# Optimization experiments

Hardware: AMD Instinct MI355X
Metric: run time of the kernel (lower is better)

Reference implementation:

```python
import jax, jax.numpy as jnp
import numpy as np

B, S, HIDDEN = 1, 2048, 2048
NUM_HEADS, MLA_DIM = 16, 128
HEAD_DIM = HIDDEN // NUM_HEADS
ROPE_BASE = 10000.0


def setup_inputs() -> dict:
    key = jax.random.key(0)
    ks = jax.random.split(key, 5)
    sd = 0.02
    hidden_states = jax.random.normal(ks[0], (B, S, HIDDEN), dtype=jnp.float32)
    wq = jax.random.normal(ks[1], (HIDDEN, NUM_HEADS * MLA_DIM), dtype=jnp.float32) * sd
    wk = jax.random.normal(ks[2], (HIDDEN, NUM_HEADS * MLA_DIM), dtype=jnp.float32) * sd
    wv = jax.random.normal(ks[3], (HIDDEN, HIDDEN), dtype=jnp.float32) * sd
    wo = jax.random.normal(ks[4], (HIDDEN, HIDDEN), dtype=jnp.float32) * sd
    # causal additive mask [B, 1, S, S]
    causal = jnp.tril(jnp.ones((S, S), dtype=bool))
    attention_mask = jnp.where(causal, 0.0, -1e9).astype(jnp.float32)[None, None]
    attention_mask = jnp.broadcast_to(attention_mask, (B, 1, S, S))
    return {"hidden_states": hidden_states, "wq": wq, "wk": wk, "wv": wv,
            "wo": wo, "attention_mask": attention_mask}


def _rope_cos_sin(seq_len, dim, dtype):
    inv_freq = 1.0 / (ROPE_BASE ** (jnp.arange(0, dim, 2, dtype=jnp.float32) / dim))
    t = jnp.arange(seq_len, dtype=jnp.float32)
    freqs = jnp.einsum('i,j->ij', t, inv_freq)           # [S, dim/2]
    emb = jnp.concatenate([freqs, freqs], axis=-1)       # [S, dim]
    cos = jnp.cos(emb)[None, :, None, :].astype(dtype)   # [1, S, 1, dim]
    sin = jnp.sin(emb)[None, :, None, :].astype(dtype)
    return cos, sin


def _rotate_half(x):
    x1, x2 = jnp.split(x, 2, axis=-1)
    return jnp.concatenate([-x2, x1], axis=-1)


def reference(hidden_states, wq, wk, wv, wo, attention_mask):
    b, s, _ = hidden_states.shape
    q = (hidden_states @ wq).reshape(b, s, NUM_HEADS, MLA_DIM)
    k = (hidden_states @ wk).reshape(b, s, NUM_HEADS, MLA_DIM)
    v = (hidden_states @ wv).reshape(b, s, NUM_HEADS, HEAD_DIM)
    cos, sin = _rope_cos_sin(s, MLA_DIM, q.dtype)
    q = q * cos + _rotate_half(q) * sin
    k = k * cos + _rotate_half(k) * sin
    scale = 1.0 / np.sqrt(MLA_DIM)
    scores = jnp.einsum('bqhd,bkhd->bhqk', q, k) * scale + attention_mask
    probs = jax.nn.softmax(scores, axis=-1)
    out = jnp.einsum('bhqk,bkhd->bqhd', probs, v).reshape(b, s, HIDDEN)
    return out @ wo
```

## Files before the change

kernel.cpp:

```cpp
#include <hip/hip_runtime.h>
#include <math.h>

namespace {

constexpr int SEQ = 2048;
constexpr int HID = 2048;
constexpr int NH  = 16;
constexpr int DH  = 128;

using f32x4  = __attribute__((ext_vector_type(4))) float;
using short8 = __attribute__((ext_vector_type(8))) short;

__device__ __forceinline__ float bflo(unsigned u) { return __uint_as_float(u << 16); }
__device__ __forceinline__ float bfhi(unsigned u) { return __uint_as_float(u & 0xFFFF0000u); }
__device__ __forceinline__ unsigned short f2bf(float f) {
    unsigned u = __float_as_uint(f);
    u += 0x7FFFu + ((u >> 16) & 1u);
    return (unsigned short)(u >> 16);
}

typedef const __attribute__((address_space(1))) unsigned int GUI;
typedef __attribute__((address_space(3))) unsigned int LUI;
__device__ __forceinline__ void async16(const void* g, void* l) {
    __builtin_amdgcn_global_load_lds((GUI*)g, (LUI*)l, 16, 0, 0);
}

__global__ __launch_bounds__(256)
void cast_bf16(const float* __restrict__ X, unsigned short* __restrict__ Y)
{
    const int i = blockIdx.x * 256 + threadIdx.x;
    const float4 v = reinterpret_cast<const float4*>(X)[i];
    ushort4 o;
    o.x = f2bf(v.x); o.y = f2bf(v.y); o.z = f2bf(v.z); o.w = f2bf(v.w);
    reinterpret_cast<ushort4*>(Y)[i] = o;
}

__global__ __launch_bounds__(256)
void transpose_cast3(const float* __restrict__ w0, const float* __restrict__ w1,
                     const float* __restrict__ w2, unsigned short* __restrict__ WT3)
{
    const int z = blockIdx.z;
    const float* W = (z == 0) ? w0 : (z == 1) ? w1 : w2;
    unsigned short* WT = WT3 + (size_t)z * HID * HID;

    __shared__ float t[32][66];
    const int tx = threadIdx.x & 31, ty = threadIdx.x >> 5;
    const int n0 = blockIdx.x * 64, k0 = blockIdx.y * 32;
    #pragma unroll
    for (int i = 0; i < 4; ++i) {
        const int kr = ty + 8 * i;
        const float2 v = *reinterpret_cast<const float2*>(
            &W[(size_t)(k0 + kr) * HID + n0 + 2 * tx]);
        t[kr][2 * tx]     = v.x;
        t[kr][2 * tx + 1] = v.y;
    }
    __syncthreads();
    #pragma unroll
    for (int i = 0; i < 8; ++i) {
        const int n = ty + 8 * i;
        WT[(size_t)(n0 + n) * HID + k0 + tx] = f2bf(t[tx][n]);
    }
}

__global__ __launch_bounds__(256)
void transpose_cast(const float* __restrict__ W, unsigned short* __restrict__ WT)
{
    __shared__ float t[32][66];
    const int tx = threadIdx.x & 31, ty = threadIdx.x >> 5;
    const int n0 = blockIdx.x * 64, k0 = blockIdx.y * 32;
    #pragma unroll
    for (int i = 0; i < 4; ++i) {
        const int kr = ty + 8 * i;
        const float2 v = *reinterpret_cast<const float2*>(
            &W[(size_t)(k0 + kr) * HID + n0 + 2 * tx]);
        t[kr][2 * tx]     = v.x;
        t[kr][2 * tx + 1] = v.y;
    }
    __syncthreads();
    #pragma unroll
    for (int i = 0; i < 8; ++i) {
        const int n = ty + 8 * i;
        WT[(size_t)(n0 + n) * HID + k0 + tx] = f2bf(t[tx][n]);
    }
}

__global__ __launch_bounds__(256)
void transp_bf16(const unsigned short* __restrict__ X, unsigned short* __restrict__ Y)
{
    __shared__ unsigned short t[32][34];
    const int tx = threadIdx.x & 31, ty = threadIdx.x >> 5;
    const int i0 = blockIdx.y * 32, j0 = blockIdx.x * 32;
    #pragma unroll
    for (int q = 0; q < 4; ++q)
        t[ty + 8 * q][tx] = X[(size_t)(i0 + ty + 8 * q) * HID + j0 + tx];
    __syncthreads();
    #pragma unroll
    for (int q = 0; q < 4; ++q)
        Y[(size_t)(j0 + ty + 8 * q) * HID + i0 + tx] = t[tx][ty + 8 * q];
}

__global__ __launch_bounds__(256)
void gemm_qkv(const unsigned short* __restrict__ A,
              const unsigned short* __restrict__ Bt3,
              unsigned short* __restrict__ Qo,
              unsigned short* __restrict__ Ko,
              unsigned short* __restrict__ Vo)
{
    __shared__ unsigned short As[128 * 64];
    __shared__ unsigned short Bs[128 * 64];

    const int tid  = threadIdx.x;
    const int lane = tid & 63;
    const int w    = tid >> 6;
    const int wr   = w >> 1, wc = w & 1;

    const int b  = blockIdx.x;
    const int sw = (b & 7) * 96 + (b >> 3);
    const int mt = sw & 15, nt = sw >> 4;
    const int m0  = mt * 128;
    const int n0g = nt * 128;
    const int wi  = nt >> 4;
    const int n0  = (nt & 15) * 128;
    unsigned short* C = (wi == 0) ? Qo : (wi == 1) ? Ko : Vo;

    const int srow = lane >> 3;
    const int sunit = lane & 7;
    const int cl = lane & 15, lg = lane >> 4;

    f32x4 acc[4][4] = {};

    for (int k0 = 0; k0 < HID; k0 += 64) {
        __syncthreads();
        #pragma unroll
        for (int i = 0; i < 4; ++i) {
            const int rb = (w * 4 + i) * 8;
            const int r  = rb + srow;
            async16(A   + (size_t)(m0  + r) * HID + k0 + sunit * 8, &As[rb * 64]);
            async16(Bt3 + (size_t)(n0g + r) * HID + k0 + sunit * 8, &Bs[rb * 64]);
        }
        __syncthreads();

        #pragma unroll
        for (int ks = 0; ks < 2; ++ks) {
            short8 af[4], bf[4];
            #pragma unroll
            for (int i = 0; i < 4; ++i) {
                af[i] = *reinterpret_cast<const short8*>(
                    &As[(wr * 64 + i * 16 + cl) * 64 + ks * 32 + lg * 8]);
                bf[i] = *reinterpret_cast<const short8*>(
                    &Bs[(wc * 64 + i * 16 + cl) * 64 + ks * 32 + lg * 8]);
            }
            #pragma unroll
            for (int i = 0; i < 4; ++i)
                #pragma unroll
                for (int j = 0; j < 4; ++j)
                    acc[i][j] = __builtin_amdgcn_mfma_f32_16x16x32_bf16(
                        af[i], bf[j], acc[i][j], 0, 0, 0);
        }
    }

    const int rg = lg * 4;
    #pragma unroll
    for (int i = 0; i < 4; ++i)
        #pragma unroll
        for (int j = 0; j < 4; ++j)
            #pragma unroll
            for (int rr = 0; rr < 4; ++rr) {
                const int row = m0 + wr * 64 + i * 16 + rg + rr;
                const int col = n0 + wc * 64 + j * 16 + cl;
                C[(size_t)row * HID + col] = f2bf(acc[i][j][rr]);
            }
}

__global__ __launch_bounds__(256)
void gemm_wo_sk(const unsigned short* __restrict__ A,
                const unsigned short* __restrict__ Bt,
                float* __restrict__ P0, float* __restrict__ P1)
{
    __shared__ unsigned short As[128 * 64];
    __shared__ unsigned short Bs[128 * 64];

    const int tid  = threadIdx.x;
    const int lane = tid & 63;
    const int w    = tid >> 6;
    const int wr   = w >> 1, wc = w & 1;

    const int b     = blockIdx.x;
    const int chunk = b >> 8;
    const int bb    = b & 255;
    const int sw = (bb & 7) * 32 + (bb >> 3);
    const int m0 = (sw >> 4) * 128, n0 = (sw & 15) * 128;
    float* C = chunk ? P1 : P0;
    const int kbase = chunk * 1024;

    const int srow = lane >> 3;
    const int sunit = lane & 7;
    const int cl = lane & 15, lg = lane >> 4;

    f32x4 acc[4][4] = {};

    for (int k0 = 0; k0 < 1024; k0 += 64) {
        __syncthreads();
        #pragma unroll
        for (int i = 0; i < 4; ++i) {
            const int rb = (w * 4 + i) * 8;
            const int r  = rb + srow;
            async16(A  + (size_t)(m0 + r) * HID + kbase + k0 + sunit * 8, &As[rb * 64]);
            async16(Bt + (size_t)(n0 + r) * HID + kbase + k0 + sunit * 8, &Bs[rb * 64]);
        }
        __syncthreads();

        #pragma unroll
        for (int ks = 0; ks < 2; ++ks) {
            short8 af[4], bf[4];
            #pragma unroll
            for (int i = 0; i < 4; ++i) {
                af[i] = *reinterpret_cast<const short8*>(
                    &As[(wr * 64 + i * 16 + cl) * 64 + ks * 32 + lg * 8]);
                bf[i] = *reinterpret_cast<const short8*>(
                    &Bs[(wc * 64 + i * 16 + cl) * 64 + ks * 32 + lg * 8]);
            }
            #pragma unroll
            for (int i = 0; i < 4; ++i)
                #pragma unroll
                for (int j = 0; j < 4; ++j)
                    acc[i][j] = __builtin_amdgcn_mfma_f32_16x16x32_bf16(
                        af[i], bf[j], acc[i][j], 0, 0, 0);
        }
    }

    const int rg = lg * 4;
    #pragma unroll
    for (int i = 0; i < 4; ++i)
        #pragma unroll
        for (int j = 0; j < 4; ++j)
            #pragma unroll
            for (int rr = 0; rr < 4; ++rr) {
                const int row = m0 + wr * 64 + i * 16 + rg + rr;
                const int col = n0 + wc * 64 + j * 16 + cl;
                C[(size_t)row * HID + col] = acc[i][j][rr];
            }
}

__global__ __launch_bounds__(256)
void reduce2(const float* __restrict__ P0, const float* __restrict__ P1,
             float* __restrict__ out)
{
    const int i = blockIdx.x * 256 + threadIdx.x;
    const float4 a = reinterpret_cast<const float4*>(P0)[i];
    const float4 b = reinterpret_cast<const float4*>(P1)[i];
    float4 r; r.x = a.x + b.x; r.y = a.y + b.y; r.z = a.z + b.z; r.w = a.w + b.w;
    reinterpret_cast<float4*>(out)[i] = r;
}

__global__ __launch_bounds__(256)
void rope_qk(unsigned short* __restrict__ Q, unsigned short* __restrict__ K)
{
    const int idx = blockIdx.x * 256 + threadIdx.x;
    const int d = idx & 63;
    const int h = (idx >> 6) & (NH - 1);
    const int s = idx >> 10;

    const float invf = exp2f(-(float)d * (13.287712379549449f / 64.0f));
    float sn, c;
    sincosf((float)s * invf, &sn, &c);

    const float SC = 0.08838834764831845f;
    const size_t base = (size_t)s * HID + h * DH + d;

    const float a0 = __uint_as_float((unsigned)Q[base]      << 16);
    const float a1 = __uint_as_float((unsigned)Q[base + 64] << 16);
    Q[base]      = f2bf((a0 * c - a1 * sn) * SC);
    Q[base + 64] = f2bf((a1 * c + a0 * sn) * SC);
    const float b0 = __uint_as_float((unsigned)K[base]      << 16);
    const float b1 = __uint_as_float((unsigned)K[base + 64] << 16);
    K[base]      = f2bf(b0 * c - b1 * sn);
    K[base + 64] = f2bf(b1 * c + b0 * sn);
}

__global__ __launch_bounds__(512, 4)
void attn_part(const unsigned short* __restrict__ Q,
               const unsigned short* __restrict__ K,
               const unsigned short* __restrict__ Vt,
               unsigned short* __restrict__ Opart,
               float2* __restrict__ ML,
               unsigned short* __restrict__ AO)
{
    __shared__ unsigned short Ks[64 * 128];
    __shared__ unsigned short Vs[128 * 64];
    __shared__ unsigned short Ps[8][16 * 72];

    const int tid  = threadIdx.x;
    const int lane = tid & 63;
    const int w    = tid >> 6;

    const int h = blockIdx.x / 30;
    int c = blockIdx.x - h * 30;
    int qb = 0;
    while (true) {
        const int cnt = (qb + 6) / 6;
        if (c < cnt) break;
        c -= cnt; ++qb;
    }
    const int cnt = (qb + 6) / 6;
    const int q0 = qb * 128;
    const int t0 = c * 12;
    const int t1 = min(2 * (qb + 1), t0 + 12);
    const bool direct = (cnt == 1);
    const int pidx = h * 24 + ((qb < 12) ? (qb - 6) * 2 : 12 + (qb - 12) * 3) + c;

    const int cl = lane & 15;
    const int lg = lane >> 4;
    const int rg = lg * 4;

    short8 aq[4];
    const unsigned short* qrow = Q + (size_t)(q0 + w * 16 + cl) * HID + h * DH;
    #pragma unroll
    for (int cc = 0; cc < 4; ++cc)
        aq[cc] = *reinterpret_cast<const short8*>(qrow + cc * 32 + lg * 8);

    f32x4 o[8] = {};
    float m[4] = {-INFINITY, -INFINITY, -INFINITY, -INFINITY};
    float l[4] = {};

    for (int t = t0; t < t1; ++t) {
        const int k0 = t * 64;

        __syncthreads();
        #pragma unroll
        for (int i = 0; i < 2; ++i) {
            const int rb = (w * 2 + i) * 4;
            const int r  = rb + (lane >> 4);
            const int gs = cl ^ (r & 7);
            async16(K + (size_t)(k0 + r) * HID + h * DH + gs * 8, &Ks[rb * 128]);
        }
        #pragma unroll
        for (int i = 0; i < 2; ++i) {
            const int rb = (w * 2 + i) * 8;
            const int r  = rb + (lane >> 3);
            const int gs = (lane & 7) ^ (r & 7);
            async16(Vt + (size_t)(h * DH + r) * SEQ + k0 + gs * 8, &Vs[rb * 64]);
        }
        __syncthreads();

        f32x4 s4[4] = {};
        __builtin_amdgcn_s_setprio(1);
        #pragma unroll
        for (int jk = 0; jk < 4; ++jk) {
            #pragma unroll
            for (int cc = 0; cc < 4; ++cc) {
                const int row  = jk * 16 + cl;
                const int slot = (cc * 4 + lg) ^ (row & 7);
                const short8 bk = *reinterpret_cast<const short8*>(
                    &Ks[row * 128 + slot * 8]);
                s4[jk] = __builtin_amdgcn_mfma_f32_16x16x32_bf16(
                    aq[cc], bk, s4[jk], 0, 0, 0);
            }
        }
        __builtin_amdgcn_s_setprio(0);

        if (t >= 2 * qb) {
            #pragma unroll
            for (int jk = 0; jk < 4; ++jk)
                #pragma unroll
                for (int r = 0; r < 4; ++r)
                    if (k0 + jk * 16 + cl > q0 + w * 16 + rg + r)
                        s4[jk][r] = -INFINITY;
        }

        float corr[4], rs[4];
        #pragma unroll
        for (int r = 0; r < 4; ++r) {
            float mx = fmaxf(fmaxf(s4[0][r], s4[1][r]),
                             fmaxf(s4[2][r], s4[3][r]));
            #pragma unroll
            for (int off = 1; off < 16; off <<= 1)
                mx = fmaxf(mx, __shfl_xor(mx, off, 64));
            const float mn = fmaxf(m[r], mx);
            corr[r] = __expf(m[r] - mn);
            m[r] = mn;
            rs[r] = 0.0f;
        }
        #pragma unroll
        for (int jk = 0; jk < 4; ++jk)
            #pragma unroll
            for (int r = 0; r < 4; ++r) {
                const float p = __expf(s4[jk][r] - m[r]);
                Ps[w][(rg + r) * 72 + jk * 16 + cl] = f2bf(p);
                rs[r] += p;
            }
        #pragma unroll
        for (int r = 0; r < 4; ++r) {
            #pragma unroll
            for (int off = 1; off < 16; off <<= 1)
                rs[r] += __shfl_xor(rs[r], off, 64);
            l[r] = l[r] * corr[r] + rs[r];
        }
        #pragma unroll
        for (int jd = 0; jd < 8; ++jd)
            #pragma unroll
            for (int r = 0; r < 4; ++r)
                o[jd][r] *= corr[r];

        __builtin_amdgcn_s_setprio(1);
        #pragma unroll
        for (int cc = 0; cc < 2; ++cc) {
            const short8 pa = *reinterpret_cast<const short8*>(
                &Ps[w][cl * 72 + cc * 32 + lg * 8]);
            #pragma unroll
            for (int jd = 0; jd < 8; ++jd) {
                const int row  = jd * 16 + cl;
                const int slot = (cc * 4 + lg) ^ (row & 7);
                const short8 bv = *reinterpret_cast<const short8*>(
                    &Vs[row * 64 + slot * 8]);
                o[jd] = __builtin_amdgcn_mfma_f32_16x16x32_bf16(
                    pa, bv, o[jd], 0, 0, 0);
            }
        }
        __builtin_amdgcn_s_setprio(0);
    }

    if (direct) {
        #pragma unroll
        for (int r = 0; r < 4; ++r) {
            const float inv = 1.0f / l[r];
            unsigned short* orow =
                AO + (size_t)(q0 + w * 16 + rg + r) * HID + h * DH;
            #pragma unroll
            for (int jd = 0; jd < 8; ++jd)
                orow[jd * 16 + cl] = f2bf(o[jd][r] * inv);
        }
    } else {
        #pragma unroll
        for (int r = 0; r < 4; ++r) {
            const int row = w * 16 + rg + r;
            if (cl == 0)
                ML[(size_t)pidx * 128 + row] = make_float2(m[r], l[r]);
            unsigned short* orow = Opart + ((size_t)pidx * 128 + row) * DH;
            #pragma unroll
            for (int jd = 0; jd < 8; ++jd)
                orow[jd * 16 + cl] = f2bf(o[jd][r]);
        }
    }
}

__global__ __launch_bounds__(256)
void attn_combine(const unsigned short* __restrict__ Opart,
                  const float2* __restrict__ ML,
                  unsigned short* __restrict__ AO)
{
    int t = blockIdx.x * 256 + threadIdx.x;
    const int dp  = t & 63;  t >>= 6;
    const int row = t & 127; t >>= 7;
    const int qq  = t % 10;
    const int h   = t / 10;
    const int qb  = 6 + qq;

    const int cnt  = (qb < 12) ? 2 : 3;
    const int base = h * 24 + ((qb < 12) ? (qb - 6) * 2 : 12 + (qb - 12) * 3);

    float mc[3], lc[3];
    unsigned uc[3];
    #pragma unroll
    for (int cc = 0; cc < 3; ++cc) {
        if (cc < cnt) {
            const int p = base + cc;
            const float2 ml = ML[(size_t)p * 128 + row];
            mc[cc] = ml.x; lc[cc] = ml.y;
            uc[cc] = reinterpret_cast<const unsigned*>(
                Opart)[((size_t)p * 128 + row) * 64 + dp];
        } else { mc[cc] = -INFINITY; lc[cc] = 0.0f; uc[cc] = 0; }
    }

    float M = fmaxf(mc[0], fmaxf(mc[1], mc[2]));
    float o0 = 0.0f, o1 = 0.0f, L = 0.0f;
    #pragma unroll
    for (int cc = 0; cc < 3; ++cc) {
        const float e = __expf(mc[cc] - M);
        o0 += bflo(uc[cc]) * e;
        o1 += bfhi(uc[cc]) * e;
        L  += lc[cc] * e;
    }

    const float inv = 1.0f / L;
    const unsigned out = (unsigned)f2bf(o0 * inv) | ((unsigned)f2bf(o1 * inv) << 16);
    const int qrow = qb * 128 + row;
    reinterpret_cast<unsigned*>(AO)[(size_t)qrow * (HID / 2) + h * (DH / 2) + dp] = out;
}

}

extern "C" void kernel_launch(void* const* d_in, const int* in_sizes, int n_in,
                              void* d_out, int out_size, void* d_ws, size_t ws_size,
                              hipStream_t stream)
{
    (void)in_sizes; (void)n_in; (void)out_size; (void)ws_size;

    const float* hs = (const float*)d_in[0];
    const float* wq = (const float*)d_in[1];
    const float* wk = (const float*)d_in[2];
    const float* wv = (const float*)d_in[3];
    const float* wo = (const float*)d_in[4];
    float* out = (float*)d_out;

    const size_t NE = (size_t)SEQ * HID;
    unsigned short* hsb = (unsigned short*)d_ws;
    unsigned short* Qb  = hsb + NE;
    unsigned short* Kb  = Qb + NE;
    unsigned short* Vb  = Kb + NE;
    unsigned short* WT3 = Vb + NE;
    unsigned short* Opart = WT3;
    float2* MLp = (float2*)(WT3 + (size_t)384 * 128 * 128);
    unsigned short* AOb = WT3 + 2 * NE;
    unsigned short* WTo = WT3;
    unsigned short* Vt  = hsb;
    float* P0 = (float*)hsb;
    float* P1 = (float*)Kb;

    cast_bf16<<<(NE / 4) / 256, 256, 0, stream>>>(hs, hsb);

    transpose_cast3<<<dim3(HID / 64, HID / 32, 3), 256, 0, stream>>>(wq, wk, wv, WT3);

    gemm_qkv<<<768, 256, 0, stream>>>(hsb, WT3, Qb, Kb, Vb);

    rope_qk<<<(SEQ * NH * 64) / 256, 256, 0, stream>>>(Qb, Kb);

    transp_bf16<<<dim3(HID / 32, HID / 32), 256, 0, stream>>>(Vb, Vt);

    attn_part<<<480, 512, 0, stream>>>(Qb, Kb, Vt, Opart, MLp, AOb);
    attn_combine<<<(16 * 10 * 128 * 64) / 256, 256, 0, stream>>>(Opart, MLp, AOb);

    transpose_cast<<<dim3(HID / 64, HID / 32), 256, 0, stream>>>(wo, WTo);
    gemm_wo_sk<<<512, 256, 0, stream>>>(AOb, WTo, P0, P1);
    reduce2<<<(int)(NE / 4 / 256), 256, 0, stream>>>(P0, P1, out);
}
```

Baseline: 345.8 us.

## Merge prep kernels, halve GEMM K-tile, read V directly from global in attention

Merges the activation cast and the three-weight transpose-cast into a single launch, using an extra z-slice for the cast. Both GEMMs drop from a 64-wide K-tile to a 32-wide one, halving shared memory per block to allow more resident blocks, at the cost of twice as many barrier pairs per K sweep. The attention kernel no longer stages V tiles in LDS and instead loads the V fragments straight from global memory for the PV MFMA. This removes LDS traffic and capacity pressure but adds uncoalesced, strided global loads inside the inner loop.

```diff
diff --git a/kernel.cpp b/kernel.cpp
--- a/kernel.cpp
+++ b/kernel.cpp
@@ -26,20 +26,24 @@
 }
 
 __global__ __launch_bounds__(256)
-void cast_bf16(const float* __restrict__ X, unsigned short* __restrict__ Y)
-{
-    const int i = blockIdx.x * 256 + threadIdx.x;
-    const float4 v = reinterpret_cast<const float4*>(X)[i];
-    ushort4 o;
-    o.x = f2bf(v.x); o.y = f2bf(v.y); o.z = f2bf(v.z); o.w = f2bf(v.w);
-    reinterpret_cast<ushort4*>(Y)[i] = o;
-}
-
-__global__ __launch_bounds__(256)
-void transpose_cast3(const float* __restrict__ w0, const float* __restrict__ w1,
-                     const float* __restrict__ w2, unsigned short* __restrict__ WT3)
+void prep(const float* __restrict__ hs,
+          const float* __restrict__ w0, const float* __restrict__ w1,
+          const float* __restrict__ w2,
+          unsigned short* __restrict__ hsb, unsigned short* __restrict__ WT3)
 {
     const int z = blockIdx.z;
+    if (z == 3) {
+        const int bid = blockIdx.y * 32 + blockIdx.x;
+        #pragma unroll
+        for (int half = 0; half < 2; ++half) {
+            const int i = bid * 256 + threadIdx.x + half * 524288;
+            const float4 v = reinterpret_cast<const float4*>(hs)[i];
+            ushort4 o;
+            o.x = f2bf(v.x); o.y = f2bf(v.y); o.z = f2bf(v.z); o.w = f2bf(v.w);
+            reinterpret_cast<ushort4*>(hsb)[i] = o;
+        }
+        return;
+    }
     const float* W = (z == 0) ? w0 : (z == 1) ? w1 : w2;
     unsigned short* WT = WT3 + (size_t)z * HID * HID;
 
@@ -106,8 +110,8 @@
               unsigned short* __restrict__ Ko,
               unsigned short* __restrict__ Vo)
 {
-    __shared__ unsigned short As[128 * 64];
-    __shared__ unsigned short Bs[128 * 64];
+    __shared__ unsigned short As[128 * 32];
+    __shared__ unsigned short Bs[128 * 32];
 
     const int tid  = threadIdx.x;
     const int lane = tid & 63;
@@ -123,43 +127,43 @@
     const int n0  = (nt & 15) * 128;
     unsigned short* C = (wi == 0) ? Qo : (wi == 1) ? Ko : Vo;
 
-    const int srow = lane >> 3;
-    const int sunit = lane & 7;
-    const int cl = lane & 15, lg = lane >> 4;
+    const int srow = lane >> 2;
+    const int scol = (lane & 3) * 8;
+    const int c0   = w * 2;
+
+    const unsigned short* gA = A   + (size_t)(m0  + c0 * 16 + srow) * HID + scol;
+    const unsigned short* gB = Bt3 + (size_t)(n0g + c0 * 16 + srow) * HID + scol;
+    unsigned short* lA = &As[c0 * 16 * 32];
+    unsigned short* lB = &Bs[c0 * 16 * 32];
 
     f32x4 acc[4][4] = {};
 
-    for (int k0 = 0; k0 < HID; k0 += 64) {
+    for (int k0 = 0; k0 < HID; k0 += 32) {
         __syncthreads();
+        async16(gA + k0,            lA);
+        async16(gA + 16 * HID + k0, lA + 16 * 32);
+        async16(gB + k0,            lB);
+        async16(gB + 16 * HID + k0, lB + 16 * 32);
+        __syncthreads();
+
+        short8 af[4], bf[4];
+        const int kb = (lane >> 4) * 8;
         #pragma unroll
         for (int i = 0; i < 4; ++i) {
-            const int rb = (w * 4 + i) * 8;
-            const int r  = rb + srow;
-            async16(A   + (size_t)(m0  + r) * HID + k0 + sunit * 8, &As[rb * 64]);
-            async16(Bt3 + (size_t)(n0g + r) * HID + k0 + sunit * 8, &Bs[rb * 64]);
-        }
-        __syncthreads();
-
-        #pragma unroll
-        for (int ks = 0; ks < 2; ++ks) {
-            short8 af[4], bf[4];
-            #pragma unroll
-            for (int i = 0; i < 4; ++i) {
-                af[i] = *reinterpret_cast<const short8*>(
-                    &As[(wr * 64 + i * 16 + cl) * 64 + ks * 32 + lg * 8]);
-                bf[i] = *reinterpret_cast<const short8*>(
-                    &Bs[(wc * 64 + i * 16 + cl) * 64 + ks * 32 + lg * 8]);
-            }
-            #pragma unroll
-            for (int i = 0; i < 4; ++i)
-                #pragma unroll
-                for (int j = 0; j < 4; ++j)
-                    acc[i][j] = __builtin_amdgcn_mfma_f32_16x16x32_bf16(
-                        af[i], bf[j], acc[i][j], 0, 0, 0);
-        }
-    }
-
-    const int rg = lg * 4;
+            af[i] = *reinterpret_cast<const short8*>(
+                &As[(wr * 64 + i * 16 + (lane & 15)) * 32 + kb]);
+            bf[i] = *reinterpret_cast<const short8*>(
+                &Bs[(wc * 64 + i * 16 + (lane & 15)) * 32 + kb]);
+        }
+        #pragma unroll
+        for (int i = 0; i < 4; ++i)
+            #pragma unroll
+            for (int j = 0; j < 4; ++j)
+                acc[i][j] = __builtin_amdgcn_mfma_f32_16x16x32_bf16(
+                    af[i], bf[j], acc[i][j], 0, 0, 0);
+    }
+
+    const int cl = lane & 15, rg = (lane >> 4) * 4;
     #pragma unroll
     for (int i = 0; i < 4; ++i)
         #pragma unroll
@@ -177,8 +181,8 @@
                 const unsigned short* __restrict__ Bt,
                 float* __restrict__ P0, float* __restrict__ P1)
 {
-    __shared__ unsigned short As[128 * 64];
-    __shared__ unsigned short Bs[128 * 64];
+    __shared__ unsigned short As[128 * 32];
+    __shared__ unsigned short Bs[128 * 32];
 
     const int tid  = threadIdx.x;
     const int lane = tid & 63;
@@ -193,43 +197,43 @@
     float* C = chunk ? P1 : P0;
     const int kbase = chunk * 1024;
 
-    const int srow = lane >> 3;
-    const int sunit = lane & 7;
-    const int cl = lane & 15, lg = lane >> 4;
+    const int srow = lane >> 2;
+    const int scol = (lane & 3) * 8;
+    const int c0   = w * 2;
+
+    const unsigned short* gA = A  + (size_t)(m0 + c0 * 16 + srow) * HID + kbase + scol;
+    const unsigned short* gB = Bt + (size_t)(n0 + c0 * 16 + srow) * HID + kbase + scol;
+    unsigned short* lA = &As[c0 * 16 * 32];
+    unsigned short* lB = &Bs[c0 * 16 * 32];
 
     f32x4 acc[4][4] = {};
 
-    for (int k0 = 0; k0 < 1024; k0 += 64) {
+    for (int k0 = 0; k0 < 1024; k0 += 32) {
         __syncthreads();
+        async16(gA + k0,            lA);
+        async16(gA + 16 * HID + k0, lA + 16 * 32);
+        async16(gB + k0,            lB);
+        async16(gB + 16 * HID + k0, lB + 16 * 32);
+        __syncthreads();
+
+        short8 af[4], bf[4];
+        const int kb = (lane >> 4) * 8;
         #pragma unroll
         for (int i = 0; i < 4; ++i) {
-            const int rb = (w * 4 + i) * 8;
-            const int r  = rb + srow;
-            async16(A  + (size_t)(m0 + r) * HID + kbase + k0 + sunit * 8, &As[rb * 64]);
-            async16(Bt + (size_t)(n0 + r) * HID + kbase + k0 + sunit * 8, &Bs[rb * 64]);
-        }
-        __syncthreads();
-
-        #pragma unroll
-        for (int ks = 0; ks < 2; ++ks) {
-            short8 af[4], bf[4];
-            #pragma unroll
-            for (int i = 0; i < 4; ++i) {
-                af[i] = *reinterpret_cast<const short8*>(
-                    &As[(wr * 64 + i * 16 + cl) * 64 + ks * 32 + lg * 8]);
-                bf[i] = *reinterpret_cast<const short8*>(
-                    &Bs[(wc * 64 + i * 16 + cl) * 64 + ks * 32 + lg * 8]);
-            }
-            #pragma unroll
-            for (int i = 0; i < 4; ++i)
-                #pragma unroll
-                for (int j = 0; j < 4; ++j)
-                    acc[i][j] = __builtin_amdgcn_mfma_f32_16x16x32_bf16(
-                        af[i], bf[j], acc[i][j], 0, 0, 0);
-        }
-    }
-
-    const int rg = lg * 4;
+            af[i] = *reinterpret_cast<const short8*>(
+                &As[(wr * 64 + i * 16 + (lane & 15)) * 32 + kb]);
+            bf[i] = *reinterpret_cast<const short8*>(
+                &Bs[(wc * 64 + i * 16 + (lane & 15)) * 32 + kb]);
+        }
+        #pragma unroll
+        for (int i = 0; i < 4; ++i)
+            #pragma unroll
+            for (int j = 0; j < 4; ++j)
+                acc[i][j] = __builtin_amdgcn_mfma_f32_16x16x32_bf16(
+                    af[i], bf[j], acc[i][j], 0, 0, 0);
+    }
+
+    const int cl = lane & 15, rg = (lane >> 4) * 4;
     #pragma unroll
     for (int i = 0; i < 4; ++i)
         #pragma unroll
@@ -287,7 +291,6 @@
                unsigned short* __restrict__ AO)
 {
     __shared__ unsigned short Ks[64 * 128];
-    __shared__ unsigned short Vs[128 * 64];
     __shared__ unsigned short Ps[8][16 * 72];
 
     const int tid  = threadIdx.x;
@@ -319,6 +322,8 @@
     for (int cc = 0; cc < 4; ++cc)
         aq[cc] = *reinterpret_cast<const short8*>(qrow + cc * 32 + lg * 8);
 
+    const unsigned short* vbase = Vt + (size_t)h * DH * SEQ;
+
     f32x4 o[8] = {};
     float m[4] = {-INFINITY, -INFINITY, -INFINITY, -INFINITY};
     float l[4] = {};
@@ -333,13 +338,6 @@
             const int r  = rb + (lane >> 4);
             const int gs = cl ^ (r & 7);
             async16(K + (size_t)(k0 + r) * HID + h * DH + gs * 8, &Ks[rb * 128]);
-        }
-        #pragma unroll
-        for (int i = 0; i < 2; ++i) {
-            const int rb = (w * 2 + i) * 8;
-            const int r  = rb + (lane >> 3);
-            const int gs = (lane & 7) ^ (r & 7);
-            async16(Vt + (size_t)(h * DH + r) * SEQ + k0 + gs * 8, &Vs[rb * 64]);
         }
         __syncthreads();
 
@@ -409,10 +407,9 @@
                 &Ps[w][cl * 72 + cc * 32 + lg * 8]);
             #pragma unroll
             for (int jd = 0; jd < 8; ++jd) {
-                const int row  = jd * 16 + cl;
-                const int slot = (cc * 4 + lg) ^ (row & 7);
+                const int row = jd * 16 + cl;
                 const short8 bv = *reinterpret_cast<const short8*>(
-                    &Vs[row * 64 + slot * 8]);
+                    vbase + (size_t)row * SEQ + k0 + cc * 32 + lg * 8);
                 o[jd] = __builtin_amdgcn_mfma_f32_16x16x32_bf16(
                     pa, bv, o[jd], 0, 0, 0);
             }
@@ -517,9 +514,7 @@
     float* P0 = (float*)hsb;
     float* P1 = (float*)Kb;
 
-    cast_bf16<<<(NE / 4) / 256, 256, 0, stream>>>(hs, hsb);
-
-    transpose_cast3<<<dim3(HID / 64, HID / 32, 3), 256, 0, stream>>>(wq, wk, wv, WT3);
+    prep<<<dim3(32, 64, 4), 256, 0, stream>>>(hs, wq, wk, wv, hsb, WT3);
 
     gemm_qkv<<<768, 256, 0, stream>>>(hsb, WT3, Qb, Kb, Vb);
 
```

Result: slower. 361.7 us (+4.6%).
